# Optimization experiments

Measured on AMD Instinct MI355X. Metric: run time of the kernel, lower is better.

Reference implementation:

```python
import jax, jax.numpy as jnp
import numpy as np

N = 4096      # nnode
F = 128       # feature_dim
E = 64        # embed_dim
P_EDGE = 0.01 # edge probability (~41 avg degree)
NEG = -9e15
ALPHA = 0.2   # leaky relu slope


def _xavier(key, shape):
    lim = float(np.sqrt(6.0 / (shape[0] + shape[1])))
    return jax.random.uniform(key, shape, minval=-lim, maxval=lim, dtype=jnp.float32)


def setup_inputs() -> dict:
    key = jax.random.key(0)
    ks = jax.random.split(key, 14)
    features = jax.random.normal(ks[0], (N, F), dtype=jnp.float32)
    eye = jnp.eye(N, dtype=jnp.float32)

    def make_adj(k):
        a = (jax.random.uniform(k, (N, N)) < P_EDGE).astype(jnp.float32)
        return jnp.maximum(a, eye)  # self loop so no empty rows

    return {
        "features": features,
        "geo_adj": make_adj(ks[1]),
        "forward_adj": make_adj(ks[2]),
        "backward_adj": make_adj(ks[3]),
        "weight": _xavier(ks[4], (E, F)),
        "Wf": _xavier(ks[5], (F, E)),
        "af1": jax.random.normal(ks[6], (E,), dtype=jnp.float32) * 0.1,
        "af2": jax.random.normal(ks[7], (E,), dtype=jnp.float32) * 0.1,
        "Wb": _xavier(ks[8], (F, E)),
        "ab1": jax.random.normal(ks[9], (E,), dtype=jnp.float32) * 0.1,
        "ab2": jax.random.normal(ks[10], (E,), dtype=jnp.float32) * 0.1,
        "Wg": _xavier(ks[11], (F, E)),
        "ag1": jax.random.normal(ks[12], (E,), dtype=jnp.float32) * 0.1,
        "ag2": jax.random.normal(ks[13], (E,), dtype=jnp.float32) * 0.1,
    }


def _mean_neighbors(adj, feat):
    # pre_weight: row-normalized neighbor averaging, (N,N) @ (N,F)
    deg = jnp.clip(jnp.sum(adj, axis=1, keepdims=True), 1.0, None)
    return (adj @ feat) / deg


def _attention(feat, mask_feat, adj, W, a1, a2):
    # GAT-style additive attention with masked softmax over neighbors
    h = feat @ W        # (N, E)
    hm = mask_feat @ W  # (N, E)
    e = jax.nn.leaky_relu((h @ a1)[:, None] + (hm @ a2)[None, :], negative_slope=ALPHA)  # (N, N)
    e = jnp.where(adj > 0, e, NEG)
    return jax.nn.softmax(e, axis=1)  # (N, N)


def reference(features, geo_adj, forward_adj, backward_adj, weight,
              Wf, af1, af2, Wb, ab1, ab2, Wg, ag1, ag2):
    t = features  # (N, F)
    mask_f = _mean_neighbors(forward_adj, t)
    mask_b = _mean_neighbors(backward_adj, t)
    mask_g = _mean_neighbors(geo_adj, t)

    w_f = _attention(t, mask_f, forward_adj, Wf, af1, af2)
    w_b = _attention(t, mask_b, backward_adj, Wb, ab1, ab2)
    w_g = _attention(t, mask_g, geo_adj, Wg, ag1, ag2)

    # get_mask_matrix_i/_j broadcast-mul + sum(1) == attn @ t (or attn.T @ t)
    x = weight @ t.T                  # (E, N)
    x_fwd = weight @ (w_f @ t).T      # mask_matrix_i
    x_bwd = weight @ (w_b.T @ t).T    # mask_matrix_j (transposed)
    x_geo = weight @ (w_g @ t).T      # mask_matrix_i

    return jnp.concatenate([x, x_fwd, x_bwd, x_geo], axis=0)  # (4E, N)
```

## Files before the change

### kernel.cpp

```cpp
#include <hip/hip_runtime.h>

#define NN 4096
#define FF 128
#define EE 64

typedef unsigned short u16;
typedef unsigned long long u64;

__device__ __forceinline__ float lrelu(float x) { return x > 0.f ? x : 0.2f * x; }

__global__ void k_prep(const float* __restrict__ Wf, const float* __restrict__ af1, const float* __restrict__ af2,
                       const float* __restrict__ Wb, const float* __restrict__ ab1, const float* __restrict__ ab2,
                       const float* __restrict__ Wg, const float* __restrict__ ag1, const float* __restrict__ ag2,
                       float* __restrict__ v6)
{
    const float* Ws[3]  = {Wf, Wb, Wg};
    const float* a1s[3] = {af1, ab1, ag1};
    const float* a2s[3] = {af2, ab2, ag2};
    int tid = threadIdx.x;
    for (int idx = tid; idx < 6 * FF; idx += 256) {
        int vi = idx >> 7, f = idx & (FF - 1), dd = vi >> 1;
        const float* a = (vi & 1) ? a2s[dd] : a1s[dd];
        const float* W = Ws[dd];
        float s = 0.f;
        for (int e = 0; e < EE; ++e) s += W[(size_t)f * EE + e] * a[e];
        v6[idx] = s;
    }
}

__global__ void k_feat(const float* __restrict__ t, const float* __restrict__ weight,
                       const float* __restrict__ v6,
                       float* __restrict__ u, float* __restrict__ s1, float* __restrict__ p,
                       float* __restrict__ out, int* __restrict__ ccnt)
{
    __shared__ __attribute__((aligned(16))) float tt[FF];
    __shared__ float vv[6 * FF];
    int n = blockIdx.x, tid = threadIdx.x;
    if (n < 16) ccnt[n * 256 + tid] = 0;
    if (tid < FF) tt[tid] = t[(size_t)n * FF + tid];
    for (int idx = tid; idx < 6 * FF; idx += 256) vv[idx] = v6[idx];
    __syncthreads();
    int e = tid >> 2, part = tid & 3;
    const float4* w4 = reinterpret_cast<const float4*>(weight + (size_t)e * FF + part * 32);
    const float4* t4 = reinterpret_cast<const float4*>(tt + part * 32);
    float s = 0.f;
    #pragma unroll
    for (int q8 = 0; q8 < 8; ++q8) {
        float4 w = w4[q8]; float4 x = t4[q8];
        s += w.x * x.x + w.y * x.y + w.z * x.z + w.w * x.w;
    }
    s += __shfl_xor(s, 1); s += __shfl_xor(s, 2);
    if (part == 0) {
        u[(size_t)n * EE + e] = s;
        out[(size_t)e * NN + n] = s;
    }
    if (tid < 64) {
        float t0 = tt[tid], t1 = tt[64 + tid];
        for (int vi = 0; vi < 6; ++vi) {
            float x = t0 * vv[vi * FF + tid] + t1 * vv[vi * FF + 64 + tid];
            for (int off = 32; off; off >>= 1) x += __shfl_xor(x, off);
            if (tid == 0) {
                int dd = vi >> 1;
                if (vi & 1) p[dd * NN + n] = x; else s1[dd * NN + n] = x;
            }
        }
    }
}

__global__ void k_mask(const float* __restrict__ Af, const float* __restrict__ Ab, const float* __restrict__ Ag,
                       u64* __restrict__ masks)
{
    int wid = threadIdx.x >> 6, lane = threadIdx.x & 63;
    int gr = blockIdx.x * 4 + wid;
    int d = gr >> 12, r = gr & (NN - 1);
    const float* A = d == 0 ? Af : (d == 1 ? Ab : Ag);
    const float4* row4 = reinterpret_cast<const float4*>(A + (size_t)r * NN);
    u64 w = 0ull;
    #pragma unroll
    for (int j = 0; j < 16; ++j) {
        float4 L = row4[j * 64 + lane];
        u64 bx = __ballot(L.x != 0.f);
        u64 by = __ballot(L.y != 0.f);
        u64 bz = __ballot(L.z != 0.f);
        u64 bw = __ballot(L.w != 0.f);
        int base = j * 4;
        if (lane == base)     w = bx;
        if (lane == base + 1) w = by;
        if (lane == base + 2) w = bz;
        if (lane == base + 3) w = bw;
    }
    masks[(size_t)gr * 64 + lane] = w;
}

__global__ void k_csr(const u64* __restrict__ masks, const float* __restrict__ p,
                      u16* __restrict__ csr, int* __restrict__ cnt, float* __restrict__ s2,
                      u16* __restrict__ csc, int* __restrict__ ccnt, int stride)
{
    int wid = threadIdx.x >> 6, lane = threadIdx.x & 63;
    int gr = blockIdx.x * 4 + wid;
    int d = gr >> 12, r = gr & (NN - 1);
    u64 m = masks[(size_t)gr * 64 + lane];
    int lc = __popcll(m);
    int sc = lc;
    for (int off = 1; off < 64; off <<= 1) {
        int o = __shfl_up(sc, off);
        if (lane >= off) sc += o;
    }
    int total = __shfl(sc, 63);
    int pos = sc - lc;
    const float* pd = p + d * NN;
    u16* crow = csr + (size_t)gr * stride;
    int colbase = (lane >> 2) * 256 + (lane & 3);
    float q = 0.f;
    while (m) {
        int b = __ffsll(m) - 1;
        m &= m - 1;
        int col = colbase + b * 4;
        if (pos < stride) crow[pos] = (u16)col;
        pos++;
        q += pd[col];
        if (d == 1) {
            int cp = atomicAdd(&ccnt[col], 1);
            if (cp < stride) csc[(size_t)col * stride + cp] = (u16)r;
        }
    }
    for (int off = 32; off; off >>= 1) q += __shfl_xor(q, off);
    if (lane == 0) {
        cnt[gr] = total;
        s2[gr] = q / fmaxf((float)total, 1.f);
    }
}

__global__ void k_zb(const float* __restrict__ s1, const float* __restrict__ s2,
                     const u16* __restrict__ csr, const int* __restrict__ cnt, int stride,
                     float* __restrict__ Zb)
{
    int tid = threadIdx.x, wave = tid >> 6, lane = tid & 63;
    int j = blockIdx.x * 4 + wave;
    int gr = NN + j;
    int nnz = min(cnt[gr], stride);
    const u16* crow = csr + (size_t)gr * stride;
    float s1j = s1[gr];
    const float* s2b = s2 + NN;
    float z = 0.f;
    if (lane < nnz)      z += __expf(lrelu(s1j + s2b[crow[lane]]));
    if (lane + 64 < nnz) z += __expf(lrelu(s1j + s2b[crow[lane + 64]]));
    for (int off = 32; off; off >>= 1) z += __shfl_xor(z, off);
    if (lane == 0) Zb[j] = z;
}

__global__ void k_out(const float* __restrict__ u,
                      const float* __restrict__ s1, const float* __restrict__ s2,
                      const float* __restrict__ Zb,
                      const u16* __restrict__ csr, const int* __restrict__ cnt,
                      const u16* __restrict__ csc, const int* __restrict__ ccnt, int stride,
                      float* __restrict__ out)
{
    __shared__ float wl[128]; __shared__ int il[128];
    __shared__ float zsum; __shared__ float oacc[4 * EE];
    int gr = blockIdx.x;
    int d = gr >> 12, i = gr & (NN - 1);
    int tid = threadIdx.x, wave = tid >> 6, lane = tid & 63;
    if (tid == 0) zsum = 0.f;
    __syncthreads();
    float invz;
    int nnz;
    if (d == 1) {
        nnz = min(ccnt[i], stride);
        const u16* ccol = csc + (size_t)i * stride;
        float s2i = s2[NN + i];
        if (tid < nnz) {
            int j = ccol[tid];
            il[tid] = j;
            wl[tid] = __expf(lrelu(s1[NN + j] + s2i)) / Zb[j];
        }
        invz = 1.f;
        __syncthreads();
    } else {
        nnz = min(cnt[gr], stride);
        const u16* crow = csr + (size_t)gr * stride;
        float s1i = s1[gr];
        const float* s2d = s2 + d * NN;
        float z = 0.f;
        if (tid < nnz) {
            int col = crow[tid];
            float w = __expf(lrelu(s1i + s2d[col]));
            il[tid] = col; wl[tid] = w; z = w;
        }
        for (int off = 32; off; off >>= 1) z += __shfl_xor(z, off);
        if (lane == 0) atomicAdd(&zsum, z);
        __syncthreads();
        float zs = zsum;
        invz = zs > 0.f ? 1.f / zs : 0.f;
    }
    float a0 = 0.f, a1 = 0.f;
    int k = wave;
    for (; k + 4 < nnz; k += 8) {
        a0 += wl[k]     * u[(size_t)il[k]     * EE + lane];
        a1 += wl[k + 4] * u[(size_t)il[k + 4] * EE + lane];
    }
    for (; k < nnz; k += 4)
        a0 += wl[k] * u[(size_t)il[k] * EE + lane];
    oacc[wave * EE + lane] = a0 + a1;
    __syncthreads();
    if (wave == 0) {
        float rsum = (oacc[lane] + oacc[EE + lane] + oacc[2 * EE + lane] + oacc[3 * EE + lane]) * invz;
        int base = 64 + (d << 6);
        out[(size_t)(base + lane) * NN + i] = rsum;
    }
}

extern "C" void kernel_launch(void* const* d_in, const int* in_sizes, int n_in,
                              void* d_out, int out_size, void* d_ws, size_t ws_size,
                              hipStream_t stream)
{
    const float* t   = (const float*)d_in[0];
    const float* Ag  = (const float*)d_in[1];
    const float* Af  = (const float*)d_in[2];
    const float* Ab  = (const float*)d_in[3];
    const float* W   = (const float*)d_in[4];
    const float* Wf  = (const float*)d_in[5];
    const float* af1 = (const float*)d_in[6];
    const float* af2 = (const float*)d_in[7];
    const float* Wb  = (const float*)d_in[8];
    const float* ab1 = (const float*)d_in[9];
    const float* ab2 = (const float*)d_in[10];
    const float* Wg  = (const float*)d_in[11];
    const float* ag1 = (const float*)d_in[12];
    const float* ag2 = (const float*)d_in[13];
    float* out = (float*)d_out;

    char* wsb = (char*)d_ws;
    u64*   masks = (u64*)wsb;
    float* v6  = (float*)(wsb + (size_t)3 * NN * 64 * 8);
    float* s1  = v6 + 6 * FF;
    float* p   = s1 + 3 * NN;
    float* s2  = p + 3 * NN;
    float* Zb  = s2 + 3 * NN;
    float* u   = Zb + NN;
    int*   cnt  = (int*)(u + (size_t)NN * EE);
    int*   ccnt = cnt + 3 * NN;
    u16*   csr  = (u16*)(ccnt + NN);

    size_t base_bytes = ((char*)csr) - wsb;
    int stride = 128;
    if (base_bytes + (size_t)4 * NN * 128 * 2 > ws_size) stride = 96;
    if (base_bytes + (size_t)4 * NN * 96 * 2 > ws_size)  stride = 64;
    u16* csc = csr + (size_t)3 * NN * stride;

    k_prep<<<1, 256, 0, stream>>>(Wf, af1, af2, Wb, ab1, ab2, Wg, ag1, ag2, v6);
    k_feat<<<NN, 256, 0, stream>>>(t, W, v6, u, s1, p, out, ccnt);
    k_mask<<<3 * NN / 4, 256, 0, stream>>>(Af, Ab, Ag, masks);
    k_csr<<<3 * NN / 4, 256, 0, stream>>>(masks, p, csr, cnt, s2, csc, ccnt, stride);
    k_zb<<<NN / 4, 256, 0, stream>>>(s1, s2, csr, cnt, stride, Zb);
    k_out<<<3 * NN, 256, 0, stream>>>(u, s1, s2, Zb, csr, cnt, csc, ccnt, stride, out);
}
```

Measured before the change: 298.7 us.

## Process four mask rows per wave and one output row per wave

```diff
diff --git a/kernel.cpp b/kernel.cpp
--- a/kernel.cpp
+++ b/kernel.cpp
@@ -67,29 +67,41 @@
     }
 }
 
-__global__ void k_mask(const float* __restrict__ Af, const float* __restrict__ Ab, const float* __restrict__ Ag,
-                       u64* __restrict__ masks)
+__global__ __launch_bounds__(256, 4)
+void k_mask(const float* __restrict__ Af, const float* __restrict__ Ab, const float* __restrict__ Ag,
+            u64* __restrict__ masks)
 {
     int wid = threadIdx.x >> 6, lane = threadIdx.x & 63;
-    int gr = blockIdx.x * 4 + wid;
-    int d = gr >> 12, r = gr & (NN - 1);
+    int wv = blockIdx.x * 4 + wid;
+    int gr0 = wv * 4;
+    int d = gr0 >> 12, r = gr0 & (NN - 1);
     const float* A = d == 0 ? Af : (d == 1 ? Ab : Ag);
-    const float4* row4 = reinterpret_cast<const float4*>(A + (size_t)r * NN);
-    u64 w = 0ull;
+    const float4* p0 = reinterpret_cast<const float4*>(A + (size_t)r * NN);
+    const float4* p1 = p0 + 1024;
+    const float4* p2 = p0 + 2048;
+    const float4* p3 = p0 + 3072;
+    u64 m0 = 0ull, m1 = 0ull, m2 = 0ull, m3 = 0ull;
     #pragma unroll
     for (int j = 0; j < 16; ++j) {
-        float4 L = row4[j * 64 + lane];
-        u64 bx = __ballot(L.x != 0.f);
-        u64 by = __ballot(L.y != 0.f);
-        u64 bz = __ballot(L.z != 0.f);
-        u64 bw = __ballot(L.w != 0.f);
+        float4 a = p0[j * 64 + lane];
+        float4 b = p1[j * 64 + lane];
+        float4 c = p2[j * 64 + lane];
+        float4 e = p3[j * 64 + lane];
         int base = j * 4;
-        if (lane == base)     w = bx;
-        if (lane == base + 1) w = by;
-        if (lane == base + 2) w = bz;
-        if (lane == base + 3) w = bw;
-    }
-    masks[(size_t)gr * 64 + lane] = w;
+#define UPD(M, L) { u64 bx = __ballot(L.x != 0.f); u64 by = __ballot(L.y != 0.f); \
+                    u64 bz = __ballot(L.z != 0.f); u64 bw = __ballot(L.w != 0.f); \
+                    if (lane == base)     M = bx; \
+                    if (lane == base + 1) M = by; \
+                    if (lane == base + 2) M = bz; \
+                    if (lane == base + 3) M = bw; }
+        UPD(m0, a) UPD(m1, b) UPD(m2, c) UPD(m3, e)
+#undef UPD
+    }
+    u64* mrow = masks + (size_t)gr0 * 64;
+    mrow[lane] = m0;
+    mrow[64 + lane] = m1;
+    mrow[128 + lane] = m2;
+    mrow[192 + lane] = m3;
 }
 
 __global__ void k_csr(const u64* __restrict__ masks, const float* __restrict__ p,
@@ -149,65 +161,61 @@
     if (lane == 0) Zb[j] = z;
 }
 
-__global__ void k_out(const float* __restrict__ u,
-                      const float* __restrict__ s1, const float* __restrict__ s2,
-                      const float* __restrict__ Zb,
-                      const u16* __restrict__ csr, const int* __restrict__ cnt,
-                      const u16* __restrict__ csc, const int* __restrict__ ccnt, int stride,
-                      float* __restrict__ out)
-{
-    __shared__ float wl[128]; __shared__ int il[128];
-    __shared__ float zsum; __shared__ float oacc[4 * EE];
-    int gr = blockIdx.x;
+__global__ __launch_bounds__(256, 4)
+void k_out(const float* __restrict__ u,
+           const float* __restrict__ s1, const float* __restrict__ s2,
+           const float* __restrict__ Zb,
+           const u16* __restrict__ csr, const int* __restrict__ cnt,
+           const u16* __restrict__ csc, const int* __restrict__ ccnt, int stride,
+           float* __restrict__ out)
+{
+    int wid = threadIdx.x >> 6, lane = threadIdx.x & 63;
+    int gr = blockIdx.x * 4 + wid;
     int d = gr >> 12, i = gr & (NN - 1);
-    int tid = threadIdx.x, wave = tid >> 6, lane = tid & 63;
-    if (tid == 0) zsum = 0.f;
-    __syncthreads();
-    float invz;
     int nnz;
+    int c0v = 0, c1v = 0;
+    float w0v = 0.f, w1v = 0.f;
     if (d == 1) {
         nnz = min(ccnt[i], stride);
-        const u16* ccol = csc + (size_t)i * stride;
+        const u16* cc = csc + (size_t)i * stride;
         float s2i = s2[NN + i];
-        if (tid < nnz) {
-            int j = ccol[tid];
-            il[tid] = j;
-            wl[tid] = __expf(lrelu(s1[NN + j] + s2i)) / Zb[j];
-        }
-        invz = 1.f;
-        __syncthreads();
+        if (lane < nnz)      { int j = cc[lane];      c0v = j; w0v = __expf(lrelu(s1[NN + j] + s2i)) / Zb[j]; }
+        if (lane + 64 < nnz) { int j = cc[lane + 64]; c1v = j; w1v = __expf(lrelu(s1[NN + j] + s2i)) / Zb[j]; }
     } else {
         nnz = min(cnt[gr], stride);
         const u16* crow = csr + (size_t)gr * stride;
         float s1i = s1[gr];
         const float* s2d = s2 + d * NN;
         float z = 0.f;
-        if (tid < nnz) {
-            int col = crow[tid];
-            float w = __expf(lrelu(s1i + s2d[col]));
-            il[tid] = col; wl[tid] = w; z = w;
-        }
+        if (lane < nnz)      { int c = crow[lane];      c0v = c; w0v = __expf(lrelu(s1i + s2d[c])); z += w0v; }
+        if (lane + 64 < nnz) { int c = crow[lane + 64]; c1v = c; w1v = __expf(lrelu(s1i + s2d[c])); z += w1v; }
         for (int off = 32; off; off >>= 1) z += __shfl_xor(z, off);
-        if (lane == 0) atomicAdd(&zsum, z);
-        __syncthreads();
-        float zs = zsum;
-        invz = zs > 0.f ? 1.f / zs : 0.f;
+        float invz = z > 0.f ? 1.f / z : 0.f;
+        w0v *= invz; w1v *= invz;
     }
     float a0 = 0.f, a1 = 0.f;
-    int k = wave;
-    for (; k + 4 < nnz; k += 8) {
-        a0 += wl[k]     * u[(size_t)il[k]     * EE + lane];
-        a1 += wl[k + 4] * u[(size_t)il[k + 4] * EE + lane];
-    }
-    for (; k < nnz; k += 4)
-        a0 += wl[k] * u[(size_t)il[k] * EE + lane];
-    oacc[wave * EE + lane] = a0 + a1;
-    __syncthreads();
-    if (wave == 0) {
-        float rsum = (oacc[lane] + oacc[EE + lane] + oacc[2 * EE + lane] + oacc[3 * EE + lane]) * invz;
-        int base = 64 + (d << 6);
-        out[(size_t)(base + lane) * NN + i] = rsum;
-    }
+    int n0 = nnz < 64 ? nnz : 64;
+    int k = 0;
+    for (; k + 1 < n0; k += 2) {
+        int ca = __shfl(c0v, k), cb = __shfl(c0v, k + 1);
+        float wa = __shfl(w0v, k), wb = __shfl(w0v, k + 1);
+        a0 += wa * u[(size_t)ca * EE + lane];
+        a1 += wb * u[(size_t)cb * EE + lane];
+    }
+    if (k < n0)
+        a0 += __shfl(w0v, k) * u[(size_t)__shfl(c0v, k) * EE + lane];
+    int n1 = nnz - 64;
+    k = 0;
+    for (; k + 1 < n1; k += 2) {
+        int ca = __shfl(c1v, k), cb = __shfl(c1v, k + 1);
+        float wa = __shfl(w1v, k), wb = __shfl(w1v, k + 1);
+        a0 += wa * u[(size_t)ca * EE + lane];
+        a1 += wb * u[(size_t)cb * EE + lane];
+    }
+    if (k < n1)
+        a0 += __shfl(w1v, k) * u[(size_t)__shfl(c1v, k) * EE + lane];
+    int base = 64 + (d << 6);
+    out[(size_t)(base + lane) * NN + i] = a0 + a1;
 }
 
 extern "C" void kernel_launch(void* const* d_in, const int* in_sizes, int n_in,
@@ -250,8 +258,8 @@
 
     k_prep<<<1, 256, 0, stream>>>(Wf, af1, af2, Wb, ab1, ab2, Wg, ag1, ag2, v6);
     k_feat<<<NN, 256, 0, stream>>>(t, W, v6, u, s1, p, out, ccnt);
-    k_mask<<<3 * NN / 4, 256, 0, stream>>>(Af, Ab, Ag, masks);
+    k_mask<<<3 * NN / 16, 256, 0, stream>>>(Af, Ab, Ag, masks);
     k_csr<<<3 * NN / 4, 256, 0, stream>>>(masks, p, csr, cnt, s2, csc, ccnt, stride);
     k_zb<<<NN / 4, 256, 0, stream>>>(s1, s2, csr, cnt, stride, Zb);
-    k_out<<<3 * NN, 256, 0, stream>>>(u, s1, s2, Zb, csr, cnt, csc, ccnt, stride, out);
-}
+    k_out<<<3 * NN / 4, 256, 0, stream>>>(u, s1, s2, Zb, csr, cnt, csc, ccnt, stride, out);
+}
```

Result: no change. 299.5 us (+0.3%).
